# Kernel tuning notes

Measured on AMD Instinct MI355X. Metric: run time of the kernel, lower is better.

Reference implementation:

```python
import jax, jax.numpy as jnp
import numpy as np


def setup_inputs() -> dict:
    key = jax.random.key(0)
    k1, k2, k3 = jax.random.split(key, 3)
    B, Cin, H, W = 64, 16, 256, 256
    Cout, K = 64, 3
    x = jax.random.normal(k1, (B, Cin, H, W), dtype=jnp.float32)
    # PyTorch Conv2d init: uniform(-s, s) with s = 1/sqrt(Cin*K*K)
    s = 1.0 / np.sqrt(Cin * K * K)
    conv_weight = jax.random.uniform(k2, (Cout, Cin, K, K), dtype=jnp.float32, minval=-s, maxval=s)
    conv_bias = jax.random.uniform(k3, (Cout,), dtype=jnp.float32, minval=-s, maxval=s)
    return {"x": x, "conv_weight": conv_weight, "conv_bias": conv_bias}


def reference(x, conv_weight, conv_bias):
    # conv2d (stride 1, no padding) -> min over channels -> tanh -> tanh
    y = jax.lax.conv_general_dilated(
        x, conv_weight,
        window_strides=(1, 1), padding='VALID',
        dimension_numbers=('NCHW', 'OIHW', 'NCHW'))
    y = y + conv_bias[None, :, None, None]          # [B, Cout, H', W']
    y = jnp.min(y, axis=1, keepdims=True)           # [B, 1, H', W']
    return jnp.tanh(jnp.tanh(y))
```

## Files before the change

kernel.cpp:

```cpp
#include <hip/hip_runtime.h>

typedef _Float16 f16x8 __attribute__((ext_vector_type(8)));
typedef _Float16 f16x2 __attribute__((ext_vector_type(2)));
typedef float    f32x4 __attribute__((ext_vector_type(4)));

#define CIN    16
#define COUT   64
#define H      256
#define W      256
#define OH     254
#define OW     254
#define TH     32
#define TW     32
#define IN_H   (TH + 2)
#define IN_W   (TW + 2)
#define IN_PIX (IN_H * IN_W)
#define NU     (IN_H * 8 * 9)

__device__ __forceinline__ float ftanh(float x) {
  float e = __expf(x + x);
  float r = __builtin_amdgcn_rcpf(e + 1.0f);
  return 1.0f - (r + r);
}

__device__ __forceinline__ f32x4 vmin4(f32x4 a, f32x4 b) {
  f32x4 r;
  r[0] = fminf(a[0], b[0]); r[1] = fminf(a[1], b[1]);
  r[2] = fminf(a[2], b[2]); r[3] = fminf(a[3], b[3]);
  return r;
}

__global__ __launch_bounds__(256, 1)
void weight_prep(const float* __restrict__ wgt, const float* __restrict__ bias,
                 _Float16* __restrict__ ws) {
  const int t = threadIdx.x;
  uint32_t* wz = (uint32_t*)(ws + 9 * COUT * 16);
  wz[t] = 0u; wz[t + 256] = 0u;
  __syncthreads();
  if (t < COUT) ws[(9 * COUT + t) * 16] = (_Float16)bias[t];
  const f32x4* w4 = (const f32x4*)wgt;
#pragma unroll
  for (int k = 0; k < 9; ++k) {
    const f32x4 v = w4[9 * t + k];
#pragma unroll
    for (int e = 0; e < 4; ++e) {
      const int g   = (9 * t + k) * 4 + e;
      const int co  = g / 144;
      const int r   = g - 144 * co;
      const int ci  = r / 9;
      const int tap = r - 9 * ci;
      ws[(tap * COUT + co) * 16 + ci] = (_Float16)v[e];
    }
  }
}

__global__ __launch_bounds__(256, 4)
void conv_min_tanh_mfma(const float* __restrict__ x, const _Float16* __restrict__ ws,
                        float* __restrict__ out) {
  __shared__ __align__(16) _Float16 xs[IN_PIX * CIN];

  const int t   = threadIdx.x;
  const int b   = blockIdx.z;
  const int ow0 = blockIdx.x * TW;
  const int oh0 = blockIdx.y * TH;

  const int lane = t & 63;
  const int ln   = lane & 15;
  const int q    = lane >> 4;
  const int qh   = q >> 1;
  const int ql   = q & 1;

  f16x8 wf[5][4];
#pragma unroll
  for (int s = 0; s < 5; ++s) {
    const int tap = 2 * s + qh;
#pragma unroll
    for (int mt = 0; mt < 4; ++mt) {
      const int cout = mt * 16 + ln;
      wf[s][mt] = *(const f16x8*)(ws + (tap * COUT + cout) * 16 + ql * 8);
    }
  }

  f16x8 cst = {};
  if (q == 2) cst[0] = (_Float16)1.0f;

  {
    f32x4 sv0[3], sv1[3];
    int   sbase[3], sj[3];
    bool  sact[3];

    auto prep = [&](int i, int slot) {
      const int  u   = t + 256 * i;
      const bool act = (u < NU);
      const int  s   = u / 9;
      const int  j   = u - 9 * s;
      const int  row = s >> 3;
      const int  cp  = s & 7;
      const int  ih  = oh0 + row;
      const int  iw0 = ow0 + 4 * j;
      const f32x4 z = {0.f, 0.f, 0.f, 0.f};
      sv0[slot] = z; sv1[slot] = z;
      if (act && ih < H && iw0 + 3 < W) {
        const float* p = x + (((size_t)b * CIN + 2 * cp) * H + ih) * W + iw0;
        sv0[slot] = *(const f32x4*)p;
        sv1[slot] = *(const f32x4*)(p + H * W);
      }
      sbase[slot] = (row * IN_W + 4 * j) * CIN + 2 * cp;
      sj[slot]    = j;
      sact[slot]  = act;
    };
    auto flush = [&](int slot) {
      if (sact[slot]) {
        const int base = sbase[slot];
        const int j    = sj[slot];
#pragma unroll
        for (int e = 0; e < 4; ++e) {
          if (4 * j + e < IN_W) {
            f16x2 h;
            h[0] = (_Float16)sv0[slot][e];
            h[1] = (_Float16)sv1[slot][e];
            *(f16x2*)(&xs[base + e * CIN]) = h;
          }
        }
      }
    };

    prep(0, 0);
    prep(1, 1);
    prep(2, 2);
#pragma unroll
    for (int i = 0; i < 10; ++i) {
      flush(i % 3);
      if (i + 3 < 10) prep(i + 3, (i + 3) % 3);
    }
  }

  int xoff[5];
#pragma unroll
  for (int s = 0; s < 5; ++s) {
    int tap = 2 * s + qh;
    if (tap > 8) tap = 8;
    const int kh = tap / 3;
    const int kw = tap - kh * 3;
    xoff[s] = (kh * IN_W + kw) * CIN + ql * 8;
  }

  __syncthreads();

  const int wv = t >> 6;
  for (int rr = 0; rr < 8; ++rr) {
    const int row = wv * 8 + rr;
#pragma unroll
    for (int ct = 0; ct < 2; ++ct) {
      const int base_idx = (row * IN_W + ct * 16 + ln) * CIN;
      f32x4 a0 = {}, a1 = {}, a2 = {}, a3 = {};
#pragma unroll
      for (int s = 0; s < 5; ++s) {
        f16x8 xf;
        if (s == 4 && qh == 1) xf = cst;
        else xf = *(const f16x8*)(&xs[base_idx + xoff[s]]);
        a0 = __builtin_amdgcn_mfma_f32_16x16x32_f16(wf[s][0], xf, a0, 0, 0, 0);
        a1 = __builtin_amdgcn_mfma_f32_16x16x32_f16(wf[s][1], xf, a1, 0, 0, 0);
        a2 = __builtin_amdgcn_mfma_f32_16x16x32_f16(wf[s][2], xf, a2, 0, 0, 0);
        a3 = __builtin_amdgcn_mfma_f32_16x16x32_f16(wf[s][3], xf, a3, 0, 0, 0);
      }
      f32x4 m4 = vmin4(vmin4(a0, a1), vmin4(a2, a3));
      float v = fminf(fminf(m4[0], m4[1]), fminf(m4[2], m4[3]));
      v = fminf(v, __shfl_xor(v, 16));
      v = fminf(v, __shfl_xor(v, 32));
      v = ftanh(ftanh(v));
      const int oh = oh0 + row;
      const int ow = ow0 + ct * 16 + ln;
      if (q == 0 && oh < OH && ow < OW)
        out[((size_t)b * OH + oh) * OW + ow] = v;
    }
  }
}

extern "C" void kernel_launch(void* const* d_in, const int* in_sizes, int n_in,
                              void* d_out, int out_size, void* d_ws, size_t ws_size,
                              hipStream_t stream) {
  const float* x    = (const float*)d_in[0];
  const float* wgt  = (const float*)d_in[1];
  const float* bias = (const float*)d_in[2];
  float* out = (float*)d_out;
  _Float16* ws = (_Float16*)d_ws;

  weight_prep<<<dim3(1, 1, 1), 256, 0, stream>>>(wgt, bias, ws);
  dim3 grid((OW + TW - 1) / TW, (OH + TH - 1) / TH, 64);
  conv_min_tanh_mfma<<<grid, 256, 0, stream>>>(x, ws, out);
}
```

Measured before the change: 418.5 us.

## Switch conv to 32x32x16 MFMA with cout split across waves and LDS min reduction

Replaces the 16x16x32 MFMA formulation, which packed two taps per instruction, with 32x32x16 MFMAs, one tap per instruction. Each pair of waves now splits the 64 output channels in halves of 32 and processes 16 rows as pairs of rows. Partial channel minima are staged in a small LDS buffer as fp16, then combined across the two waves before tanh and the store, with barriers added per phase. This aims to cut LDS fragment reloads and shuffle overhead per output. The cost is extra synchronization and rounding the intermediate min to fp16, which reduces precision.

Result: faster. 391.4 us (-6.5%).

```diff
diff --git a/kernel.cpp b/kernel.cpp
--- a/kernel.cpp
+++ b/kernel.cpp
@@ -3,6 +3,7 @@
 typedef _Float16 f16x8 __attribute__((ext_vector_type(8)));
 typedef _Float16 f16x2 __attribute__((ext_vector_type(2)));
 typedef float    f32x4 __attribute__((ext_vector_type(4)));
+typedef float    f32x16 __attribute__((ext_vector_type(16)));
 
 #define CIN    16
 #define COUT   64
@@ -30,6 +31,15 @@
   return r;
 }
 
+__device__ __forceinline__ float rmin16(const f32x16& A) {
+  f32x4 a = {A[0], A[1], A[2], A[3]};
+  f32x4 b = {A[4], A[5], A[6], A[7]};
+  f32x4 c = {A[8], A[9], A[10], A[11]};
+  f32x4 d = {A[12], A[13], A[14], A[15]};
+  f32x4 m = vmin4(vmin4(a, b), vmin4(c, d));
+  return fminf(fminf(m[0], m[1]), fminf(m[2], m[3]));
+}
+
 __global__ __launch_bounds__(256, 1)
 void weight_prep(const float* __restrict__ wgt, const float* __restrict__ bias,
                  _Float16* __restrict__ ws) {
@@ -58,6 +68,7 @@
 void conv_min_tanh_mfma(const float* __restrict__ x, const _Float16* __restrict__ ws,
                         float* __restrict__ out) {
   __shared__ __align__(16) _Float16 xs[IN_PIX * CIN];
+  __shared__ _Float16 sm[2][16][32];
 
   const int t   = threadIdx.x;
   const int b   = blockIdx.z;
@@ -65,24 +76,19 @@
   const int oh0 = blockIdx.y * TH;
 
   const int lane = t & 63;
-  const int ln   = lane & 15;
-  const int q    = lane >> 4;
-  const int qh   = q >> 1;
-  const int ql   = q & 1;
-
-  f16x8 wf[5][4];
-#pragma unroll
-  for (int s = 0; s < 5; ++s) {
-    const int tap = 2 * s + qh;
-#pragma unroll
-    for (int mt = 0; mt < 4; ++mt) {
-      const int cout = mt * 16 + ln;
-      wf[s][mt] = *(const f16x8*)(ws + (tap * COUT + cout) * 16 + ql * 8);
-    }
-  }
+  const int n32  = lane & 31;
+  const int hl   = lane >> 5;
+  const int wv   = t >> 6;
+  const int ch   = wv & 1;
+  const int pr   = wv >> 1;
+
+  f16x8 wf[10];
+#pragma unroll
+  for (int tp = 0; tp < 10; ++tp)
+    wf[tp] = *(const f16x8*)(ws + (tp * COUT + ch * 32 + n32) * 16 + hl * 8);
 
   f16x8 cst = {};
-  if (q == 2) cst[0] = (_Float16)1.0f;
+  if (hl == 0) cst[0] = (_Float16)1.0f;
 
   {
     f32x4 sv0[3], sv1[3];
@@ -135,45 +141,48 @@
     }
   }
 
-  int xoff[5];
-#pragma unroll
-  for (int s = 0; s < 5; ++s) {
-    int tap = 2 * s + qh;
-    if (tap > 8) tap = 8;
-    const int kh = tap / 3;
-    const int kw = tap - kh * 3;
-    xoff[s] = (kh * IN_W + kw) * CIN + ql * 8;
-  }
-
   __syncthreads();
 
-  const int wv = t >> 6;
-  for (int rr = 0; rr < 8; ++rr) {
-    const int row = wv * 8 + rr;
-#pragma unroll
-    for (int ct = 0; ct < 2; ++ct) {
-      const int base_idx = (row * IN_W + ct * 16 + ln) * CIN;
-      f32x4 a0 = {}, a1 = {}, a2 = {}, a3 = {};
-#pragma unroll
-      for (int s = 0; s < 5; ++s) {
-        f16x8 xf;
-        if (s == 4 && qh == 1) xf = cst;
-        else xf = *(const f16x8*)(&xs[base_idx + xoff[s]]);
-        a0 = __builtin_amdgcn_mfma_f32_16x16x32_f16(wf[s][0], xf, a0, 0, 0, 0);
-        a1 = __builtin_amdgcn_mfma_f32_16x16x32_f16(wf[s][1], xf, a1, 0, 0, 0);
-        a2 = __builtin_amdgcn_mfma_f32_16x16x32_f16(wf[s][2], xf, a2, 0, 0, 0);
-        a3 = __builtin_amdgcn_mfma_f32_16x16x32_f16(wf[s][3], xf, a3, 0, 0, 0);
-      }
-      f32x4 m4 = vmin4(vmin4(a0, a1), vmin4(a2, a3));
-      float v = fminf(fminf(m4[0], m4[1]), fminf(m4[2], m4[3]));
-      v = fminf(v, __shfl_xor(v, 16));
-      v = fminf(v, __shfl_xor(v, 32));
-      v = ftanh(ftanh(v));
-      const int oh = oh0 + row;
-      const int ow = ow0 + ct * 16 + ln;
-      if (q == 0 && oh < OH && ow < OW)
+  for (int ph = 0; ph < 2; ++ph) {
+#pragma unroll
+    for (int rp = 0; rp < 4; ++rp) {
+      const int r0 = pr * 16 + ph * 8 + rp * 2;
+      const _Float16* p0 = xs + (r0 * IN_W + n32) * CIN + hl * 8;
+      const _Float16* p1 = p0 + IN_W * CIN;
+      f32x16 A0 = {}, A1 = {};
+#pragma unroll
+      for (int tp = 0; tp < 9; ++tp) {
+        const int off = ((tp / 3) * IN_W + (tp % 3)) * CIN;
+        f16x8 x0 = *(const f16x8*)(p0 + off);
+        f16x8 x1 = *(const f16x8*)(p1 + off);
+        A0 = __builtin_amdgcn_mfma_f32_32x32x16_f16(wf[tp], x0, A0, 0, 0, 0);
+        A1 = __builtin_amdgcn_mfma_f32_32x32x16_f16(wf[tp], x1, A1, 0, 0, 0);
+      }
+      A0 = __builtin_amdgcn_mfma_f32_32x32x16_f16(wf[9], cst, A0, 0, 0, 0);
+      A1 = __builtin_amdgcn_mfma_f32_32x32x16_f16(wf[9], cst, A1, 0, 0, 0);
+      float v0 = rmin16(A0), v1 = rmin16(A1);
+      v0 = fminf(v0, __shfl_xor(v0, 32));
+      v1 = fminf(v1, __shfl_xor(v1, 32));
+      if (lane < 32) {
+        sm[ch][pr * 8 + rp * 2 + 0][lane] = (_Float16)v0;
+        sm[ch][pr * 8 + rp * 2 + 1][lane] = (_Float16)v1;
+      }
+    }
+    __syncthreads();
+
+#pragma unroll
+    for (int k2 = 0; k2 < 2; ++k2) {
+      const int r = wv * 4 + hl * 2 + k2;
+      const float s0 = (float)sm[0][r][n32];
+      const float s1 = (float)sm[1][r][n32];
+      const float v  = ftanh(ftanh(fminf(s0, s1)));
+      const int orow = (r >> 3) * 16 + ph * 8 + (r & 7);
+      const int oh = oh0 + orow;
+      const int ow = ow0 + n32;
+      if (oh < OH && ow < OW)
         out[((size_t)b * OH + oh) * OW + ow] = v;
     }
+    __syncthreads();
   }
 }
 
```
